# Kernel tuning notes

Measured on AMD Instinct MI355X. Metric: run time of the kernel, lower is better.

The kernel has to match this reference:

```python
import jax, jax.numpy as jnp
import numpy as np

B, C, F_, T = 32, 2, 1024, 512
CF = C * F_
H = 128  # lstm hidden / embedding dim


def setup_inputs() -> dict:
    key = jax.random.key(0)
    ks = jax.random.split(key, 12)
    s = 0.05
    return {
        "x": jax.random.normal(ks[0], (B, C, F_, T), dtype=jnp.float32),
        "W_fc1": jax.random.normal(ks[1], (H, CF), dtype=jnp.float32) * s,
        "b_fc1": jax.random.normal(ks[2], (H,), dtype=jnp.float32) * s,
        "Wih_f": jax.random.normal(ks[3], (4 * H, H), dtype=jnp.float32) * s,
        "Whh_f": jax.random.normal(ks[4], (4 * H, H), dtype=jnp.float32) * s,
        "b_f": jax.random.normal(ks[5], (4 * H,), dtype=jnp.float32) * s,
        "Wih_b": jax.random.normal(ks[6], (4 * H, H), dtype=jnp.float32) * s,
        "Whh_b": jax.random.normal(ks[7], (4 * H, H), dtype=jnp.float32) * s,
        "b_b": jax.random.normal(ks[8], (4 * H,), dtype=jnp.float32) * s,
        "W_out": jax.random.normal(ks[9], (H, 2 * H), dtype=jnp.float32) * s,
        "b_out": jax.random.normal(ks[10], (H,), dtype=jnp.float32) * s,
    }


def _lstm_scan(x, Wih, Whh, b):
    # x: (L, T, H); recurrence over L (torch treats the (B,128) input as an
    # unbatched sequence of length B), vectorized over the T frames.
    L, Tn, _ = x.shape
    Hn = Whh.shape[1]

    def step(carry, xt):
        h, c = carry  # (T, H)
        z = xt @ Wih.T + h @ Whh.T + b  # (T, 4H)
        i, f, g, o = jnp.split(z, 4, axis=-1)
        c = jax.nn.sigmoid(f) * c + jax.nn.sigmoid(i) * jnp.tanh(g)
        h = jax.nn.sigmoid(o) * jnp.tanh(c)
        return (h, c), h

    init = (jnp.zeros((Tn, Hn), x.dtype), jnp.zeros((Tn, Hn), x.dtype))
    _, hs = jax.lax.scan(step, init, x)
    return hs  # (L, T, H)


def reference(x, W_fc1, b_fc1, Wih_f, Whh_f, b_f, Wih_b, Whh_b, b_b, W_out, b_out):
    Bn, Cn, Fn, Tn = x.shape
    # fc1 applied per time frame: (B, CF, T) -> (B, T, 128)
    xr = x.reshape(Bn, Cn * Fn, Tn).transpose(0, 2, 1)
    h = jnp.einsum("btc,dc->btd", xr, W_fc1) + b_fc1
    # bidirectional LSTM over the batch axis (torch unbatched-input semantics)
    hf = _lstm_scan(h, Wih_f, Whh_f, b_f)
    hb = _lstm_scan(h[::-1], Wih_b, Whh_b, b_b)[::-1]
    hs = jnp.concatenate([hf, hb], axis=-1)  # (B, T, 256)
    out = jnp.einsum("btd,ed->bte", hs, W_out) + b_out  # (B, T, 128)
    return out.transpose(0, 2, 1)  # (B, 128, T), matching torch.stack(dim=2)
```

## Files before the change

### kernel.cpp

```cpp
#include <hip/hip_runtime.h>
#include <stdint.h>

typedef __attribute__((ext_vector_type(8))) short short8;
typedef __attribute__((ext_vector_type(4))) float floatx4;

__device__ __forceinline__ float bf16_to_f(uint16_t u) {
    union { uint32_t i; float f; } v; v.i = ((uint32_t)u) << 16; return v.f;
}
__device__ __forceinline__ uint16_t f_to_bf16(float f) {
    union { uint32_t i; float f; } v; v.f = f;
    uint32_t u = v.i;
    u += 0x7FFFu + ((u >> 16) & 1u);
    return (uint16_t)(u >> 16);
}
__device__ __forceinline__ void gload16(const void* g, void* l) {
    __builtin_amdgcn_global_load_lds(
        (const __attribute__((address_space(1))) void*)g,
        (__attribute__((address_space(3))) void*)l, 16, 0, 0);
}
__device__ __forceinline__ float rcpf(float x) { return __builtin_amdgcn_rcpf(x); }

__device__ __forceinline__ void bar_lds() {
    asm volatile("s_waitcnt lgkmcnt(0)" ::: "memory");
    __builtin_amdgcn_s_barrier();
    asm volatile("" ::: "memory");
}

#define B_  32
#define T_  512
#define CF_ 2048
#define H_  128
#define G4_ 512
#define LOG2E 1.4426950408889634f

__global__ __launch_bounds__(256) void k_cvt_all(
        const float* __restrict__ Wfc, const float* __restrict__ Wih_f,
        const float* __restrict__ Wih_b, const float* __restrict__ Whh_f,
        const float* __restrict__ Whh_b, const float* __restrict__ Wout,
        uint16_t* __restrict__ WfcB, uint16_t* __restrict__ WihB,
        uint16_t* __restrict__ WhhB, uint16_t* __restrict__ WoutB) {
    const int blk = blockIdx.x;
    const float* s; uint16_t* d; int off;
    if (blk < 256)      { s = Wfc;   d = WfcB;          off = blk; }
    else if (blk < 320) { s = Wih_f; d = WihB;          off = blk - 256; }
    else if (blk < 384) { s = Wih_b; d = WihB + 65536;  off = blk - 320; }
    else if (blk < 448) { s = Whh_f; d = WhhB;          off = blk - 384; }
    else if (blk < 512) { s = Whh_b; d = WhhB + 65536;  off = blk - 448; }
    else                { s = Wout;  d = WoutB;         off = blk - 512; }
    const int i = off * 1024 + threadIdx.x * 4;
    float4 v = *(const float4*)&s[i];
    ushort4 o;
    o.x = f_to_bf16(v.x); o.y = f_to_bf16(v.y);
    o.z = f_to_bf16(v.z); o.w = f_to_bf16(v.w);
    *(ushort4*)&d[i] = o;
}

__global__ __launch_bounds__(512) void k_fc1x(const float* __restrict__ x,
                                              const uint16_t* __restrict__ WfcB,
                                              const float* __restrict__ bfc,
                                              const uint16_t* __restrict__ WihB,
                                              const float* __restrict__ b_f,
                                              const float* __restrict__ b_b,
                                              uint16_t* __restrict__ Xp) {
    __shared__ float tile[64 * 65];
    __shared__ __align__(16) uint16_t As[8192];
    __shared__ __align__(16) uint16_t Bs[4224];
    __shared__ __align__(16) uint16_t Hs2[8432];

    const int bb = blockIdx.y, n0 = blockIdx.x * 64;
    const int tid = threadIdx.x, w = tid >> 6, l = tid & 63;
    const int lm = l & 15, lk = l >> 4;
    const float* xb = x + (size_t)bb * CF_ * T_;

    const int t4 = (tid & 15) * 4, cf_r = tid >> 4;
    const int kk = (tid & 15) * 4, t_r = tid >> 4;

    float4 xv0, xv1;
    {
        const float* p = &xb[(size_t)(0 + cf_r) * T_ + n0 + t4];
        xv0 = *(const float4*)p;
        xv1 = *(const float4*)(p + 32 * T_);
    }

    const int wmA = (w >> 1) * 32, wnA = (w & 1) * 32;
    floatx4 acc[2][2] = {};
    for (int k0 = 0; k0 < CF_; k0 += 64) {
        __syncthreads();
        tile[(t4 + 0) * 65 + cf_r] = xv0.x;
        tile[(t4 + 1) * 65 + cf_r] = xv0.y;
        tile[(t4 + 2) * 65 + cf_r] = xv0.z;
        tile[(t4 + 3) * 65 + cf_r] = xv0.w;
        tile[(t4 + 0) * 65 + cf_r + 32] = xv1.x;
        tile[(t4 + 1) * 65 + cf_r + 32] = xv1.y;
        tile[(t4 + 2) * 65 + cf_r + 32] = xv1.z;
        tile[(t4 + 3) * 65 + cf_r + 32] = xv1.w;
        gload16(WfcB + (size_t)l * CF_ + k0 + w * 8,        As + (w * 128 + l) * 8);
        gload16(WfcB + (size_t)(64 + l) * CF_ + k0 + w * 8, As + (w * 128 + 64 + l) * 8);
        __syncthreads();
        if (k0 + 64 < CF_) {
            const float* p = &xb[(size_t)(k0 + 64 + cf_r) * T_ + n0 + t4];
            xv0 = *(const float4*)p;
            xv1 = *(const float4*)(p + 32 * T_);
        }
        #pragma unroll
        for (int pass = 0; pass < 2; ++pass) {
            const int tr = t_r + pass * 32;
            ushort4 o;
            o.x = f_to_bf16(tile[tr * 65 + kk + 0]);
            o.y = f_to_bf16(tile[tr * 65 + kk + 1]);
            o.z = f_to_bf16(tile[tr * 65 + kk + 2]);
            o.w = f_to_bf16(tile[tr * 65 + kk + 3]);
            *(ushort4*)&Bs[((kk >> 3) * 66 + tr) * 8 + (kk & 7)] = o;
        }
        __syncthreads();
        short8 a[2][2], bfr[2][2];
        #pragma unroll
        for (int kf = 0; kf < 2; ++kf) {
            #pragma unroll
            for (int mf = 0; mf < 2; ++mf)
                a[mf][kf] = *(const short8*)&As[((kf * 4 + lk) * 128 + wmA + mf * 16 + lm) * 8];
            #pragma unroll
            for (int nf = 0; nf < 2; ++nf)
                bfr[nf][kf] = *(const short8*)&Bs[((kf * 4 + lk) * 66 + wnA + nf * 16 + lm) * 8];
        }
        #pragma unroll
        for (int mf = 0; mf < 2; ++mf)
            #pragma unroll
            for (int nf = 0; nf < 2; ++nf) {
                acc[mf][nf] = __builtin_amdgcn_mfma_f32_16x16x32_bf16(a[mf][0], bfr[nf][0], acc[mf][nf], 0, 0, 0);
                acc[mf][nf] = __builtin_amdgcn_mfma_f32_16x16x32_bf16(a[mf][1], bfr[nf][1], acc[mf][nf], 0, 0, 0);
            }
    }
    __syncthreads();
    #pragma unroll
    for (int mf = 0; mf < 2; ++mf) {
        const int d0 = wmA + mf * 16 + lk * 4;
        const float4 bv = *(const float4*)&bfc[d0];
        const int c = ((wmA + mf * 16) >> 3) + (lk >> 1);
        #pragma unroll
        for (int nf = 0; nf < 2; ++nf) {
            const int t = wnA + nf * 16 + lm;
            ushort4 o;
            o.x = f_to_bf16(acc[mf][nf][0] + bv.x);
            o.y = f_to_bf16(acc[mf][nf][1] + bv.y);
            o.z = f_to_bf16(acc[mf][nf][2] + bv.z);
            o.w = f_to_bf16(acc[mf][nf][3] + bv.w);
            *(ushort4*)&Hs2[(c * 66 + t) * 8 + (lk & 1) * 4] = o;
        }
    }
    __syncthreads();

    const int dirw = w >> 2;
    const int db   = dirw * B_ + bb;
    const uint16_t* Wp = WihB + (size_t)dirw * (G4_ * H_);
    const float* bi = dirw ? b_b : b_f;
    #pragma unroll
    for (int it = 0; it < 2; ++it) {
        const int gbase = (w & 3) * 64 + it * 256;
        short8 aw[4][4];
        #pragma unroll
        for (int mf = 0; mf < 4; ++mf)
            #pragma unroll
            for (int kf = 0; kf < 4; ++kf)
                aw[mf][kf] = *(const short8*)&Wp[(size_t)(gbase + mf * 16 + lm) * H_ + kf * 32 + lk * 8];
        floatx4 acc2[4][4] = {};
        #pragma unroll
        for (int nf = 0; nf < 4; ++nf) {
            short8 bbf[4];
            #pragma unroll
            for (int kf = 0; kf < 4; ++kf)
                bbf[kf] = *(const short8*)&Hs2[((kf * 4 + lk) * 66 + nf * 16 + lm) * 8];
            #pragma unroll
            for (int mf = 0; mf < 4; ++mf)
                #pragma unroll
                for (int kf = 0; kf < 4; ++kf)
                    acc2[mf][nf] = __builtin_amdgcn_mfma_f32_16x16x32_bf16(aw[mf][kf], bbf[kf], acc2[mf][nf], 0, 0, 0);
        }
        #pragma unroll
        for (int mf = 0; mf < 4; ++mf) {
            const int g0 = gbase + mf * 16 + lk * 4;
            const float4 bv = *(const float4*)&bi[g0];
            #pragma unroll
            for (int nf = 0; nf < 4; ++nf) {
                const int t = n0 + nf * 16 + lm;
                ushort4 o;
                o.x = f_to_bf16(acc2[mf][nf][0] + bv.x);
                o.y = f_to_bf16(acc2[mf][nf][1] + bv.y);
                o.z = f_to_bf16(acc2[mf][nf][2] + bv.z);
                o.w = f_to_bf16(acc2[mf][nf][3] + bv.w);
                *(ushort4*)&Xp[((size_t)db * T_ + t) * G4_ + g0] = o;
            }
        }
    }
}

__global__ __launch_bounds__(512) void k_lstm(const uint16_t* __restrict__ Xp,
                                              const uint16_t* __restrict__ WhhB,
                                              uint16_t* __restrict__ hs) {
    __shared__ __align__(16) uint16_t h_sh[2][16 * 136];
    const int dir = blockIdx.y, t0 = blockIdx.x * 16;
    const int tid = threadIdx.x, w = tid >> 6, l = tid & 63;
    const int lm = l & 15, lk = l >> 4;
    const int gcol = w * 16 + lm;
    const int tloc = lk * 4;
    const uint16_t* Wp = WhhB + dir * (G4_ * H_);

    short8 bw[4][4];
    #pragma unroll
    for (int q = 0; q < 4; ++q)
        #pragma unroll
        for (int kf = 0; kf < 4; ++kf)
            bw[q][kf] = *(const short8*)&Wp[(size_t)(q * H_ + gcol) * H_ + kf * 32 + lk * 8];

    for (int i = tid; i < 16 * 136; i += 512) h_sh[0][i] = 0;
    float c[4] = {0.f, 0.f, 0.f, 0.f};

    uint16_t xva[4][4], xvb[4][4];
    {
        const int b0 = dir ? (B_ - 1) : 0;
        const uint16_t* xp = Xp + ((size_t)(dir * B_ + b0) * T_ + t0 + tloc) * G4_;
        #pragma unroll
        for (int r = 0; r < 4; ++r)
            #pragma unroll
            for (int q = 0; q < 4; ++q)
                xva[r][q] = xp[(size_t)r * G4_ + q * H_ + gcol];
    }
    bar_lds();

    auto step = [&](int s, uint16_t (&xc)[4][4], uint16_t (&xn)[4][4], int par) {
        const int b_idx = dir ? (B_ - 1 - s) : s;
        short8 af[4];
        #pragma unroll
        for (int kf = 0; kf < 4; ++kf)
            af[kf] = *(const short8*)&h_sh[par][lm * 136 + kf * 32 + lk * 8];
        floatx4 acc[4] = {};
        #pragma unroll
        for (int q = 0; q < 4; ++q)
            #pragma unroll
            for (int kf = 0; kf < 4; ++kf)
                acc[q] = __builtin_amdgcn_mfma_f32_16x16x32_bf16(af[kf], bw[q][kf], acc[q], 0, 0, 0);
        if (s < B_ - 1) {
            const int bn = dir ? (B_ - 2 - s) : (s + 1);
            const uint16_t* xp = Xp + ((size_t)(dir * B_ + bn) * T_ + t0 + tloc) * G4_;
            #pragma unroll
            for (int r = 0; r < 4; ++r)
                #pragma unroll
                for (int q = 0; q < 4; ++q)
                    xn[r][q] = xp[(size_t)r * G4_ + q * H_ + gcol];
        }
        #pragma unroll
        for (int r = 0; r < 4; ++r) {
            float zi = acc[0][r] + bf16_to_f(xc[r][0]);
            float zf = acc[1][r] + bf16_to_f(xc[r][1]);
            float zg = acc[2][r] + bf16_to_f(xc[r][2]);
            float zo = acc[3][r] + bf16_to_f(xc[r][3]);
            float si = rcpf(1.f + __builtin_amdgcn_exp2f(-LOG2E * zi));
            float sf = rcpf(1.f + __builtin_amdgcn_exp2f(-LOG2E * zf));
            float so = rcpf(1.f + __builtin_amdgcn_exp2f(-LOG2E * zo));
            float tg = 1.f - 2.f * rcpf(1.f + __builtin_amdgcn_exp2f(2.f * LOG2E * zg));
            c[r] = sf * c[r] + si * tg;
            float tc = 1.f - 2.f * rcpf(1.f + __builtin_amdgcn_exp2f(2.f * LOG2E * c[r]));
            float hn = so * tc;
            uint16_t hb = f_to_bf16(hn);
            h_sh[par ^ 1][(tloc + r) * 136 + gcol] = hb;
            hs[((size_t)b_idx * T_ + t0 + tloc + r) * 256 + dir * H_ + gcol] = hb;
        }
        bar_lds();
    };

    for (int s2 = 0; s2 < 16; ++s2) {
        step(2 * s2,     xva, xvb, 0);
        step(2 * s2 + 1, xvb, xva, 1);
    }
}

__global__ __launch_bounds__(256) void k_outm(const uint16_t* __restrict__ WoutB,
                                              const uint16_t* __restrict__ hs,
                                              const float* __restrict__ bout,
                                              float* __restrict__ out) {
    __shared__ __align__(16) uint16_t As[4096], Bs[4096];
    const int b = blockIdx.z, m0 = blockIdx.y * 64, n0 = blockIdx.x * 64;
    const int tid = threadIdx.x, w = tid >> 6, l = tid & 63;
    const int wm = (w >> 1) * 32, wn = (w & 1) * 32;
    const int lm = l & 15, lk = l >> 4;
    const uint16_t* A = WoutB + (size_t)m0 * 256;
    const uint16_t* Bp = hs + ((size_t)b * T_ + n0) * 256;
    floatx4 acc[2][2] = {};
    const uint16_t* gA = A + (size_t)l * 256;
    const uint16_t* gB = Bp + (size_t)l * 256;
    for (int k0 = 0; k0 < 256; k0 += 64) {
        __syncthreads();
        gload16(gA + k0 + (2 * w) * 8,     As + ((2 * w) * 64 + l) * 8);
        gload16(gA + k0 + (2 * w + 1) * 8, As + ((2 * w + 1) * 64 + l) * 8);
        gload16(gB + k0 + (2 * w) * 8,     Bs + ((2 * w) * 64 + l) * 8);
        gload16(gB + k0 + (2 * w + 1) * 8, Bs + ((2 * w + 1) * 64 + l) * 8);
        __syncthreads();
        short8 a[2][2], bfr[2][2];
        #pragma unroll
        for (int kf = 0; kf < 2; ++kf) {
            #pragma unroll
            for (int mf = 0; mf < 2; ++mf)
                a[mf][kf] = *(const short8*)&As[((kf * 4 + lk) * 64 + wm + mf * 16 + lm) * 8];
            #pragma unroll
            for (int nf = 0; nf < 2; ++nf)
                bfr[nf][kf] = *(const short8*)&Bs[((kf * 4 + lk) * 64 + wn + nf * 16 + lm) * 8];
        }
        #pragma unroll
        for (int mf = 0; mf < 2; ++mf)
            #pragma unroll
            for (int nf = 0; nf < 2; ++nf) {
                acc[mf][nf] = __builtin_amdgcn_mfma_f32_16x16x32_bf16(a[mf][0], bfr[nf][0], acc[mf][nf], 0, 0, 0);
                acc[mf][nf] = __builtin_amdgcn_mfma_f32_16x16x32_bf16(a[mf][1], bfr[nf][1], acc[mf][nf], 0, 0, 0);
            }
    }
    #pragma unroll
    for (int mf = 0; mf < 2; ++mf) {
        const int e0 = m0 + wm + mf * 16 + lk * 4;
        const float4 bv = *(const float4*)&bout[e0];
        #pragma unroll
        for (int nf = 0; nf < 2; ++nf) {
            const int t = n0 + wn + nf * 16 + lm;
            out[((size_t)b * H_ + e0 + 0) * T_ + t] = acc[mf][nf][0] + bv.x;
            out[((size_t)b * H_ + e0 + 1) * T_ + t] = acc[mf][nf][1] + bv.y;
            out[((size_t)b * H_ + e0 + 2) * T_ + t] = acc[mf][nf][2] + bv.z;
            out[((size_t)b * H_ + e0 + 3) * T_ + t] = acc[mf][nf][3] + bv.w;
        }
    }
}

extern "C" void kernel_launch(void* const* d_in, const int* in_sizes, int n_in,
                              void* d_out, int out_size, void* d_ws, size_t ws_size,
                              hipStream_t stream) {
    const float* x     = (const float*)d_in[0];
    const float* Wfc   = (const float*)d_in[1];
    const float* bfc   = (const float*)d_in[2];
    const float* Wih_f = (const float*)d_in[3];
    const float* Whh_f = (const float*)d_in[4];
    const float* b_f   = (const float*)d_in[5];
    const float* Wih_b = (const float*)d_in[6];
    const float* Whh_b = (const float*)d_in[7];
    const float* b_b   = (const float*)d_in[8];
    const float* Wout  = (const float*)d_in[9];
    const float* bout  = (const float*)d_in[10];
    float* out = (float*)d_out;

    char* ws = (char*)d_ws;
    uint16_t* Xp    = (uint16_t*)(ws);
    uint16_t* hsB   = (uint16_t*)(ws + 33554432);
    uint16_t* WfcB  = (uint16_t*)(ws + 41943040);
    uint16_t* WihB  = (uint16_t*)(ws + 42467328);
    uint16_t* WhhB  = (uint16_t*)(ws + 42729472);
    uint16_t* WoutB = (uint16_t*)(ws + 42991616);

    k_cvt_all<<<dim3(544), 256, 0, stream>>>(Wfc, Wih_f, Wih_b, Whh_f, Whh_b, Wout,
                                             WfcB, WihB, WhhB, WoutB);
    k_fc1x <<<dim3(8, 32),   512, 0, stream>>>(x, WfcB, bfc, WihB, b_f, b_b, Xp);
    k_lstm <<<dim3(32, 2),   512, 0, stream>>>(Xp, WhhB, hsB);
    k_outm <<<dim3(8, 2, 32), 256, 0, stream>>>(WoutB, hsB, bout, out);
}
```

Before: 278.9 us.

## Split fc1 GEMM over K and move input projection to separate kernel

Splits the fc1 reduction over the 2048 input channels into four chunks so four times as many blocks run, writes fp32 partials, and sums them with bias in a new reduction kernel. The LSTM input projection is moved out of the fc1 kernel into its own tiled MFMA GEMM. This aims to raise occupancy and parallelism in the front stage. The trade-off is extra global traffic for the partial sums and intermediate buffer, plus two more kernel launches.

```diff
diff --git a/kernel.cpp b/kernel.cpp
--- a/kernel.cpp
+++ b/kernel.cpp
@@ -31,6 +31,7 @@
 #define CF_ 2048
 #define H_  128
 #define G4_ 512
+#define BT_ 16384
 #define LOG2E 1.4426950408889634f
 
 __global__ __launch_bounds__(256) void k_cvt_all(
@@ -55,19 +56,15 @@
     *(ushort4*)&d[i] = o;
 }
 
-__global__ __launch_bounds__(512) void k_fc1x(const float* __restrict__ x,
+__global__ __launch_bounds__(512) void k_fc1a(const float* __restrict__ x,
                                               const uint16_t* __restrict__ WfcB,
-                                              const float* __restrict__ bfc,
-                                              const uint16_t* __restrict__ WihB,
-                                              const float* __restrict__ b_f,
-                                              const float* __restrict__ b_b,
-                                              uint16_t* __restrict__ Xp) {
+                                              float* __restrict__ Hpart) {
     __shared__ float tile[64 * 65];
     __shared__ __align__(16) uint16_t As[8192];
     __shared__ __align__(16) uint16_t Bs[4224];
-    __shared__ __align__(16) uint16_t Hs2[8432];
-
-    const int bb = blockIdx.y, n0 = blockIdx.x * 64;
+
+    const int bb = blockIdx.y, n0 = blockIdx.x * 64, kc = blockIdx.z;
+    const int kbase = kc * 512;
     const int tid = threadIdx.x, w = tid >> 6, l = tid & 63;
     const int lm = l & 15, lk = l >> 4;
     const float* xb = x + (size_t)bb * CF_ * T_;
@@ -77,14 +74,15 @@
 
     float4 xv0, xv1;
     {
-        const float* p = &xb[(size_t)(0 + cf_r) * T_ + n0 + t4];
+        const float* p = &xb[(size_t)(kbase + cf_r) * T_ + n0 + t4];
         xv0 = *(const float4*)p;
         xv1 = *(const float4*)(p + 32 * T_);
     }
 
     const int wmA = (w >> 1) * 32, wnA = (w & 1) * 32;
     floatx4 acc[2][2] = {};
-    for (int k0 = 0; k0 < CF_; k0 += 64) {
+    for (int i = 0; i < 8; ++i) {
+        const int k0 = kbase + i * 64;
         __syncthreads();
         tile[(t4 + 0) * 65 + cf_r] = xv0.x;
         tile[(t4 + 1) * 65 + cf_r] = xv0.y;
@@ -97,7 +95,7 @@
         gload16(WfcB + (size_t)l * CF_ + k0 + w * 8,        As + (w * 128 + l) * 8);
         gload16(WfcB + (size_t)(64 + l) * CF_ + k0 + w * 8, As + (w * 128 + 64 + l) * 8);
         __syncthreads();
-        if (k0 + 64 < CF_) {
+        if (i < 7) {
             const float* p = &xb[(size_t)(k0 + 64 + cf_r) * T_ + n0 + t4];
             xv0 = *(const float4*)p;
             xv1 = *(const float4*)(p + 32 * T_);
@@ -131,65 +129,106 @@
                 acc[mf][nf] = __builtin_amdgcn_mfma_f32_16x16x32_bf16(a[mf][1], bfr[nf][1], acc[mf][nf], 0, 0, 0);
             }
     }
-    __syncthreads();
+    float* Hp = Hpart + (size_t)kc * H_ * BT_;
     #pragma unroll
     for (int mf = 0; mf < 2; ++mf) {
         const int d0 = wmA + mf * 16 + lk * 4;
-        const float4 bv = *(const float4*)&bfc[d0];
-        const int c = ((wmA + mf * 16) >> 3) + (lk >> 1);
         #pragma unroll
         for (int nf = 0; nf < 2; ++nf) {
-            const int t = wnA + nf * 16 + lm;
+            const int bt = bb * T_ + n0 + wnA + nf * 16 + lm;
+            #pragma unroll
+            for (int r = 0; r < 4; ++r)
+                Hp[(size_t)(d0 + r) * BT_ + bt] = acc[mf][nf][r];
+        }
+    }
+}
+
+__global__ __launch_bounds__(256) void k_hsum(const float* __restrict__ Hpart,
+                                              const float* __restrict__ bfc,
+                                              uint16_t* __restrict__ Hcm) {
+    const int d = blockIdx.y, bt = blockIdx.x * 1024 + threadIdx.x * 4;
+    const float b = bfc[d];
+    float4 s = *(const float4*)&Hpart[(size_t)d * BT_ + bt];
+    #pragma unroll
+    for (int kc = 1; kc < 4; ++kc) {
+        const float4 v = *(const float4*)&Hpart[(size_t)kc * H_ * BT_ + (size_t)d * BT_ + bt];
+        s.x += v.x; s.y += v.y; s.z += v.z; s.w += v.w;
+    }
+    uint16_t* o = Hcm + ((size_t)(d >> 3) * BT_ + bt) * 8 + (d & 7);
+    o[0]  = f_to_bf16(s.x + b);
+    o[8]  = f_to_bf16(s.y + b);
+    o[16] = f_to_bf16(s.z + b);
+    o[24] = f_to_bf16(s.w + b);
+}
+
+__global__ __launch_bounds__(256) void k_xproj(const uint16_t* __restrict__ Hcm,
+                                               const uint16_t* __restrict__ WihB,
+                                               const float* __restrict__ b_f,
+                                               const float* __restrict__ b_b,
+                                               uint16_t* __restrict__ Xp) {
+    __shared__ __align__(16) uint16_t As[64 * 136];
+    __shared__ __align__(16) uint16_t Bs[16 * 66 * 8];
+    const int bt0 = blockIdx.x * 64, gy = blockIdx.y;
+    const int dir = gy >> 3;
+    const int gl0 = gy * 64 - dir * 512;
+    const int tid = threadIdx.x, w = tid >> 6, l = tid & 63;
+    const int lm = l & 15, lk = l >> 4;
+
+    #pragma unroll
+    for (int j = 0; j < 4; ++j) {
+        const int c = w * 4 + j;
+        gload16(Hcm + ((size_t)c * BT_ + bt0 + l) * 8, Bs + (c * 66 + l) * 8);
+    }
+    {
+        const int r = tid >> 2, c4 = tid & 3;
+        const uint16_t* src = WihB + (size_t)(gy * 64 + r) * H_ + c4 * 32;
+        short8 v0 = *(const short8*)(src);
+        short8 v1 = *(const short8*)(src + 8);
+        short8 v2 = *(const short8*)(src + 16);
+        short8 v3 = *(const short8*)(src + 24);
+        uint16_t* dst = &As[r * 136 + c4 * 32];
+        *(short8*)(dst)      = v0;
+        *(short8*)(dst + 8)  = v1;
+        *(short8*)(dst + 16) = v2;
+        *(short8*)(dst + 24) = v3;
+    }
+    __syncthreads();
+
+    const int wm = (w >> 1) * 32, wn = (w & 1) * 32;
+    short8 a[2][4], bfr[2][4];
+    #pragma unroll
+    for (int kf = 0; kf < 4; ++kf) {
+        #pragma unroll
+        for (int mf = 0; mf < 2; ++mf)
+            a[mf][kf] = *(const short8*)&As[(wm + mf * 16 + lm) * 136 + kf * 32 + lk * 8];
+        #pragma unroll
+        for (int nf = 0; nf < 2; ++nf)
+            bfr[nf][kf] = *(const short8*)&Bs[((kf * 4 + lk) * 66 + wn + nf * 16 + lm) * 8];
+    }
+    floatx4 acc[2][2] = {};
+    #pragma unroll
+    for (int kf = 0; kf < 4; ++kf)
+        #pragma unroll
+        for (int mf = 0; mf < 2; ++mf)
+            #pragma unroll
+            for (int nf = 0; nf < 2; ++nf)
+                acc[mf][nf] = __builtin_amdgcn_mfma_f32_16x16x32_bf16(a[mf][kf], bfr[nf][kf], acc[mf][nf], 0, 0, 0);
+
+    const float* bi = dir ? b_b : b_f;
+    #pragma unroll
+    for (int mf = 0; mf < 2; ++mf) {
+        const int g = gl0 + wm + mf * 16 + lk * 4;
+        const float4 bv = *(const float4*)&bi[g];
+        #pragma unroll
+        for (int nf = 0; nf < 2; ++nf) {
+            const int bt = bt0 + wn + nf * 16 + lm;
+            const int bb = bt >> 9, t = bt & 511;
             ushort4 o;
             o.x = f_to_bf16(acc[mf][nf][0] + bv.x);
             o.y = f_to_bf16(acc[mf][nf][1] + bv.y);
             o.z = f_to_bf16(acc[mf][nf][2] + bv.z);
             o.w = f_to_bf16(acc[mf][nf][3] + bv.w);
-            *(ushort4*)&Hs2[(c * 66 + t) * 8 + (lk & 1) * 4] = o;
-        }
-    }
-    __syncthreads();
-
-    const int dirw = w >> 2;
-    const int db   = dirw * B_ + bb;
-    const uint16_t* Wp = WihB + (size_t)dirw * (G4_ * H_);
-    const float* bi = dirw ? b_b : b_f;
-    #pragma unroll
-    for (int it = 0; it < 2; ++it) {
-        const int gbase = (w & 3) * 64 + it * 256;
-        short8 aw[4][4];
-        #pragma unroll
-        for (int mf = 0; mf < 4; ++mf)
-            #pragma unroll
-            for (int kf = 0; kf < 4; ++kf)
-                aw[mf][kf] = *(const short8*)&Wp[(size_t)(gbase + mf * 16 + lm) * H_ + kf * 32 + lk * 8];
-        floatx4 acc2[4][4] = {};
-        #pragma unroll
-        for (int nf = 0; nf < 4; ++nf) {
-            short8 bbf[4];
-            #pragma unroll
-            for (int kf = 0; kf < 4; ++kf)
-                bbf[kf] = *(const short8*)&Hs2[((kf * 4 + lk) * 66 + nf * 16 + lm) * 8];
-            #pragma unroll
-            for (int mf = 0; mf < 4; ++mf)
-                #pragma unroll
-                for (int kf = 0; kf < 4; ++kf)
-                    acc2[mf][nf] = __builtin_amdgcn_mfma_f32_16x16x32_bf16(aw[mf][kf], bbf[kf], acc2[mf][nf], 0, 0, 0);
-        }
-        #pragma unroll
-        for (int mf = 0; mf < 4; ++mf) {
-            const int g0 = gbase + mf * 16 + lk * 4;
-            const float4 bv = *(const float4*)&bi[g0];
-            #pragma unroll
-            for (int nf = 0; nf < 4; ++nf) {
-                const int t = n0 + nf * 16 + lm;
-                ushort4 o;
-                o.x = f_to_bf16(acc2[mf][nf][0] + bv.x);
-                o.y = f_to_bf16(acc2[mf][nf][1] + bv.y);
-                o.z = f_to_bf16(acc2[mf][nf][2] + bv.z);
-                o.w = f_to_bf16(acc2[mf][nf][3] + bv.w);
-                *(ushort4*)&Xp[((size_t)db * T_ + t) * G4_ + g0] = o;
-            }
+            *(ushort4*)&Xp[((size_t)(dir * B_ + bb) * T_ + t) * G4_ + g] = o;
         }
     }
 }
@@ -347,14 +386,18 @@
     char* ws = (char*)d_ws;
     uint16_t* Xp    = (uint16_t*)(ws);
     uint16_t* hsB   = (uint16_t*)(ws + 33554432);
-    uint16_t* WfcB  = (uint16_t*)(ws + 41943040);
-    uint16_t* WihB  = (uint16_t*)(ws + 42467328);
-    uint16_t* WhhB  = (uint16_t*)(ws + 42729472);
-    uint16_t* WoutB = (uint16_t*)(ws + 42991616);
+    float*    Hpart = (float*)   (ws + 41943040);
+    uint16_t* Hcm   = (uint16_t*)(ws + 75497472);
+    uint16_t* WfcB  = (uint16_t*)(ws + 79691776);
+    uint16_t* WihB  = (uint16_t*)(ws + 80216064);
+    uint16_t* WhhB  = (uint16_t*)(ws + 80478208);
+    uint16_t* WoutB = (uint16_t*)(ws + 80740352);
 
     k_cvt_all<<<dim3(544), 256, 0, stream>>>(Wfc, Wih_f, Wih_b, Whh_f, Whh_b, Wout,
                                              WfcB, WihB, WhhB, WoutB);
-    k_fc1x <<<dim3(8, 32),   512, 0, stream>>>(x, WfcB, bfc, WihB, b_f, b_b, Xp);
-    k_lstm <<<dim3(32, 2),   512, 0, stream>>>(Xp, WhhB, hsB);
+    k_fc1a <<<dim3(8, 32, 4), 512, 0, stream>>>(x, WfcB, Hpart);
+    k_hsum <<<dim3(16, 128),  256, 0, stream>>>(Hpart, bfc, Hcm);
+    k_xproj<<<dim3(256, 16),  256, 0, stream>>>(Hcm, WihB, b_f, b_b, Xp);
+    k_lstm <<<dim3(32, 2),    512, 0, stream>>>(Xp, WhhB, hsB);
     k_outm <<<dim3(8, 2, 32), 256, 0, stream>>>(WoutB, hsB, bout, out);
 }
```

Result: slower. 300.8 us (+7.8%).
